# Optimization experiments

Measured on AMD Instinct MI355X. Metric: run time of the kernel, lower is better.

The kernel has to match this reference:

```python
import jax, jax.numpy as jnp
import numpy as np

N = 2048      # num_nodes
K = 8         # Chebyshev order
HEADS = 4
BETA = 0.5
EPS = 1e-6


def setup_inputs() -> dict:
    key = jax.random.key(0)
    ks = jax.random.split(key, 5)
    # edge_index enumerates all ordered node pairs i != j (row-major), matching
    # the [2, N*(N-1)] logits parameter layout of the module.
    ii, jj = np.meshgrid(np.arange(N), np.arange(N), indexing='ij')
    mask = ii != jj
    edge_index = jnp.asarray(np.stack([ii[mask], jj[mask]]), dtype=jnp.int32)  # [2, E]
    E = N * (N - 1)
    logits = jax.random.normal(ks[0], (2, E), dtype=jnp.float32)
    s = 1.0 / np.sqrt(K)
    w0 = jax.random.normal(ks[1], (HEADS, K), dtype=jnp.float32) * s  # Linear(K,1) weight per head
    b0 = jax.random.normal(ks[2], (HEADS,), dtype=jnp.float32) * s
    w1 = jax.random.normal(ks[3], (HEADS, K), dtype=jnp.float32) * s
    b1 = jax.random.normal(ks[4], (HEADS,), dtype=jnp.float32) * s
    return {"edge_index": edge_index, "logits": logits, "w0": w0, "b0": b0, "w1": w1, "b1": b1}


def _laplacian(vals, src, dst, dtype):
    # to_dense_adj + L = -D^{-1/2} A D^{-1/2}, with diag matmuls as broadcast scaling
    A = jnp.zeros((N, N), dtype).at[src, dst].add(vals)
    dinv = 1.0 / jnp.sqrt(A.sum(axis=1) + EPS)
    return -(dinv[:, None] * A) * dinv[None, :]


def _cheb_gather(L, src, dst):
    # T1 = L, Tk = 2 L Tkm1 - Tkm2; gather edge entries of T1..TK -> [E, K]
    cols = [L[src, dst]]
    Tkm2 = jnp.eye(N, dtype=L.dtype)
    Tkm1 = L
    for _ in range(K - 1):
        Tk = 2.0 * (L @ Tkm1) - Tkm2
        cols.append(Tk[src, dst])
        Tkm2, Tkm1 = Tkm1, Tk
    return jnp.stack(cols, axis=1)


def reference(edge_index, logits, w0, b0, w1, b1):
    src, dst = edge_index[0], edge_index[1]
    edge_prob = jax.nn.softmax(BETA * logits, axis=0)  # softmax over the 2 branches
    L0 = _laplacian(edge_prob[0], src, dst, logits.dtype)
    L1 = _laplacian(edge_prob[1], src, dst, logits.dtype)
    Lks0 = _cheb_gather(L0, src, dst)  # [E, K]
    Lks1 = _cheb_gather(L1, src, dst)  # [E, K]
    f0 = (Lks0 @ w0.T + b0).T  # [heads, E], theta0[i](Lks0).squeeze(-1)
    f1 = (Lks1 @ w1.T + b1).T  # [heads, E]
    return edge_prob, f0, f1
```

## Files before the change

### kernel.cpp

```cpp
#include <hip/hip_runtime.h>
#include <math.h>

#define NN 2048
#define NM1 2047
#define EDGES (NN * NM1)
#define KORD 8
#define NHEADS 4
#define BETA 0.5f
#define EPSV 1e-6f

typedef __attribute__((ext_vector_type(8))) short bf16x8;
typedef __attribute__((ext_vector_type(4))) float f32x4;

__device__ __forceinline__ unsigned short f2bf(float f) {
    unsigned u = __builtin_bit_cast(unsigned, f);
    u += 0x7FFF + ((u >> 16) & 1);
    return (unsigned short)(u >> 16);
}
__device__ __forceinline__ float bf2f(unsigned short h) {
    unsigned u = ((unsigned)h) << 16;
    return __builtin_bit_cast(float, u);
}

#define GLD16(gp, lp) __builtin_amdgcn_global_load_lds(                         \
    (const __attribute__((address_space(1))) void*)(gp),                        \
    (__attribute__((address_space(3))) void*)(lp), 16, 0, 0)

__global__ void k_prob(const float* __restrict__ logits, float* __restrict__ out) {
    int e = blockIdx.x * 256 + threadIdx.x;
    if (e >= EDGES) return;
    float l0 = logits[e];
    float l1 = logits[EDGES + e];
    float p0 = 1.f / (1.f + __expf(BETA * (l1 - l0)));
    float p1 = 1.f / (1.f + __expf(BETA * (l0 - l1)));
    out[e]         = p0;
    out[EDGES + e] = p1;
}

__global__ __launch_bounds__(256) void k_dinv(const float* __restrict__ out, float* __restrict__ dinv) {
    int row = blockIdx.x, br = blockIdx.y;
    const float* p = out + (size_t)br * EDGES + (size_t)row * NM1;
    float s = 0.f;
    for (int t = threadIdx.x; t < NM1; t += 256) s += p[t];
    for (int off = 32; off; off >>= 1) s += __shfl_down(s, off);
    __shared__ float red[4];
    if ((threadIdx.x & 63) == 0) red[threadIdx.x >> 6] = s;
    __syncthreads();
    if (threadIdx.x == 0)
        dinv[br * NN + row] = 1.f / sqrtf(red[0] + red[1] + red[2] + red[3] + EPSV);
}

__global__ __launch_bounds__(256) void k_build(const float* __restrict__ out, const float* __restrict__ dinv,
                                               unsigned short* __restrict__ Lb0, unsigned short* __restrict__ Lb1) {
    int idx = blockIdx.x * 256 + threadIdx.x;
    int br = blockIdx.y;
    int i = idx >> 11, j = idx & (NN - 1);
    unsigned short* Lb = br ? Lb1 : Lb0;
    float v = 0.f;
    if (i != j) {
        float pp = out[(size_t)br * EDGES + (size_t)i * NM1 + (j < i ? j : j - 1)];
        v = -dinv[br * NN + i] * pp * dinv[br * NN + j];
    }
    Lb[idx] = f2bf(v);
}

__global__ __launch_bounds__(256) void k_transpose(
    const unsigned short* __restrict__ S0, const unsigned short* __restrict__ S1,
    unsigned short* __restrict__ D0, unsigned short* __restrict__ D1) {
    __shared__ unsigned short T[64 * 66];
    const unsigned short* S = blockIdx.z ? S1 : S0;
    unsigned short* D = blockIdx.z ? D1 : D0;
    int t = threadIdx.x;
    int I0 = blockIdx.y * 64, J0 = blockIdx.x * 64;
    int r = t >> 2, cb = (t & 3) * 16;
    {
        const uint4* src = (const uint4*)(S + (size_t)(I0 + r) * NN + J0 + cb);
        uint4 v0 = src[0], v1 = src[1];
        unsigned* d = (unsigned*)&T[r * 66 + cb];
        d[0] = v0.x; d[1] = v0.y; d[2] = v0.z; d[3] = v0.w;
        d[4] = v1.x; d[5] = v1.y; d[6] = v1.z; d[7] = v1.w;
    }
    __syncthreads();
    union { unsigned short u[16]; uint4 q[2]; } pk;
#pragma unroll
    for (int q = 0; q < 16; ++q) pk.u[q] = T[(cb + q) * 66 + r];
    unsigned short* dst = D + (size_t)(J0 + r) * NN + I0 + cb;
    ((uint4*)dst)[0] = pk.q[0];
    ((uint4*)dst)[1] = pk.q[1];
}

__global__ __launch_bounds__(256) void k_cheb(
    const unsigned short* __restrict__ A0, const unsigned short* __restrict__ A1,
    const unsigned short* __restrict__ B0, const unsigned short* __restrict__ B1,
    const unsigned short* __restrict__ P0, const unsigned short* __restrict__ P1,
    unsigned short* __restrict__ O0, unsigned short* __restrict__ O1, int first) {
    __shared__ unsigned short As[128 * 32];
    __shared__ unsigned short Bs[128 * 32];
    const int z = blockIdx.z;
    const unsigned short* A   = z ? A1 : A0;
    const unsigned short* BT  = z ? B1 : B0;
    const unsigned short* Um2 = z ? P1 : P0;
    unsigned short* Un        = z ? O1 : O0;

    int tid = threadIdx.x;
    int w = tid >> 6, l = tid & 63;
    int wr = w >> 1, wc = w & 1;
    int r0 = blockIdx.y * 128, c0 = blockIdx.x * 128;

    int srow = l >> 2;
    int schk = ((l & 3) ^ ((l >> 3) & 3)) * 8;
    const unsigned short* ga  = A  + (size_t)(r0 + w * 16 + srow) * NN + schk;
    const unsigned short* gb  = BT + (size_t)(c0 + w * 16 + srow) * NN + schk;
    const unsigned short* ga2 = ga + (size_t)64 * NN;
    const unsigned short* gb2 = gb + (size_t)64 * NN;
    unsigned short* lA  = As + w * 512;
    unsigned short* lA2 = As + 2048 + w * 512;
    unsigned short* lB  = Bs + w * 512;
    unsigned short* lB2 = Bs + 2048 + w * 512;

    f32x4 acc[4][4] = {};
    int lr = l & 15, g = l >> 4;
    int rchk = (g ^ ((lr >> 1) & 3)) * 8;

    for (int k0 = 0; k0 < NN; k0 += 32) {
        __syncthreads();
        GLD16(ga + k0, lA);
        GLD16(ga2 + k0, lA2);
        GLD16(gb + k0, lB);
        GLD16(gb2 + k0, lB2);
        __syncthreads();
        bf16x8 af[4], bf[4];
#pragma unroll
        for (int m = 0; m < 4; ++m)
            af[m] = *(const bf16x8*)(As + (wr * 64 + m * 16 + lr) * 32 + rchk);
#pragma unroll
        for (int n = 0; n < 4; ++n)
            bf[n] = *(const bf16x8*)(Bs + (wc * 64 + n * 16 + lr) * 32 + rchk);
#pragma unroll
        for (int m = 0; m < 4; ++m)
#pragma unroll
            for (int n = 0; n < 4; ++n)
                acc[m][n] = __builtin_amdgcn_mfma_f32_16x16x32_bf16(af[m], bf[n], acc[m][n], 0, 0, 0);
    }

#pragma unroll
    for (int m = 0; m < 4; ++m)
#pragma unroll
        for (int n = 0; n < 4; ++n)
#pragma unroll
            for (int r = 0; r < 4; ++r) {
                int row = r0 + wr * 64 + m * 16 + g * 4 + r;
                int col = c0 + wc * 64 + n * 16 + lr;
                size_t off = (size_t)row * NN + col;
                float prev = first ? (row == col ? 1.f : 0.f) : bf2f(Um2[off]);
                Un[off] = f2bf(2.f * acc[m][n][r] - prev);
            }
}

__global__ __launch_bounds__(256) void k_gather(
    const unsigned short* __restrict__ Lb,
    const unsigned short* __restrict__ U2, const unsigned short* __restrict__ U3,
    const unsigned short* __restrict__ U4, const unsigned short* __restrict__ U5,
    const unsigned short* __restrict__ U6, const unsigned short* __restrict__ U7,
    const unsigned short* __restrict__ U8,
    const float* __restrict__ w, const float* __restrict__ bias,
    float* __restrict__ fout) {
    __shared__ unsigned short G[64 * 66];
    int t = threadIdx.x;
    int I0 = blockIdx.y * 64, J0 = blockIdx.x * 64;
    int jo = t & 63, ig = t >> 6;
    int sr = t >> 2, scb = (t & 3) * 16;

    float acc[4][16];
#pragma unroll
    for (int h = 0; h < 4; ++h)
#pragma unroll
        for (int s = 0; s < 16; ++s) acc[h][s] = 0.f;

    const unsigned short* mats[8] = {Lb, U2, U3, U4, U5, U6, U7, U8};
#pragma unroll
    for (int kk = 0; kk < 8; ++kk) {
        const unsigned short* M = mats[kk];
        int R0 = (kk == 0) ? I0 : J0;
        int C0 = (kk == 0) ? J0 : I0;
        __syncthreads();
        {
            const uint4* src = (const uint4*)(M + (size_t)(R0 + sr) * NN + C0 + scb);
            uint4 v0 = src[0], v1 = src[1];
            unsigned* d = (unsigned*)&G[sr * 66 + scb];
            d[0] = v0.x; d[1] = v0.y; d[2] = v0.z; d[3] = v0.w;
            d[4] = v1.x; d[5] = v1.y; d[6] = v1.z; d[7] = v1.w;
        }
        __syncthreads();
        float c0w = w[0 * KORD + kk], c1w = w[1 * KORD + kk];
        float c2w = w[2 * KORD + kk], c3w = w[3 * KORD + kk];
#pragma unroll
        for (int s = 0; s < 16; ++s) {
            int io = ig * 16 + s;
            unsigned short raw = (kk == 0) ? G[io * 66 + jo] : G[jo * 66 + io];
            float v = bf2f(raw);
            acc[0][s] += c0w * v;
            acc[1][s] += c1w * v;
            acc[2][s] += c2w * v;
            acc[3][s] += c3w * v;
        }
    }
    float b0v = bias[0], b1v = bias[1], b2v = bias[2], b3v = bias[3];
#pragma unroll
    for (int s = 0; s < 16; ++s) {
        int i = I0 + ig * 16 + s;
        int j = J0 + jo;
        if (i == j) continue;
        size_t e = (size_t)i * NM1 + (j < i ? j : j - 1);
        fout[0 * (size_t)EDGES + e] = b0v + acc[0][s];
        fout[1 * (size_t)EDGES + e] = b1v + acc[1][s];
        fout[2 * (size_t)EDGES + e] = b2v + acc[2][s];
        fout[3 * (size_t)EDGES + e] = b3v + acc[3][s];
    }
}

extern "C" void kernel_launch(void* const* d_in, const int* in_sizes, int n_in,
                              void* d_out, int out_size, void* d_ws, size_t ws_size,
                              hipStream_t stream) {
    const float* logits = (const float*)d_in[1];
    const float* w0 = (const float*)d_in[2];
    const float* b0 = (const float*)d_in[3];
    const float* w1 = (const float*)d_in[4];
    const float* b1 = (const float*)d_in[5];
    float* out = (float*)d_out;

    char* ws = (char*)d_ws;
    const size_t MATB = (size_t)NN * NN * sizeof(unsigned short);
    unsigned short* Lb0 = (unsigned short*)(ws);
    unsigned short* Lb1 = (unsigned short*)(ws + MATB);
    unsigned short* U0[9];
    for (int k = 2; k <= 8; ++k) U0[k] = (unsigned short*)(ws + (size_t)k * MATB);
    float* dinv = (float*)(ws + 9 * MATB);
    unsigned short* obase = (unsigned short*)(out + 2 * (size_t)EDGES);
    unsigned short* U1[9];
    for (int k = 2; k <= 8; ++k) U1[k] = obase + (size_t)(k - 2) * NN * NN;
    unsigned short* LT0 = U0[8];
    unsigned short* LT1 = U1[8];

    k_prob<<<(EDGES + 255) / 256, 256, 0, stream>>>(logits, out);
    k_dinv<<<dim3(NN, 2), 256, 0, stream>>>(out, dinv);
    k_build<<<dim3((NN * NN) / 256, 2), 256, 0, stream>>>(out, dinv, Lb0, Lb1);
    k_transpose<<<dim3(32, 32, 2), 256, 0, stream>>>(Lb0, Lb1, LT0, LT1);

    for (int n = 2; n <= 8; ++n) {
        const unsigned short* A0p = (n == 2) ? LT0 : U0[n - 1];
        const unsigned short* A1p = (n == 2) ? LT1 : U1[n - 1];
        const unsigned short* P0p = (n <= 3) ? LT0 : U0[n - 2];
        const unsigned short* P1p = (n <= 3) ? LT1 : U1[n - 2];
        k_cheb<<<dim3(16, 16, 2), 256, 0, stream>>>(A0p, A1p, Lb0, Lb1, P0p, P1p,
                                                    U0[n], U1[n], (n == 2) ? 1 : 0);
    }

    float* f1 = out + 2 * (size_t)EDGES + 4 * (size_t)EDGES;
    k_gather<<<dim3(32, 32), 256, 0, stream>>>(Lb1, U1[2], U1[3], U1[4], U1[5], U1[6], U1[7], U1[8],
                                               w1, b1, f1);
    float* f0 = out + 2 * (size_t)EDGES;
    k_gather<<<dim3(32, 32), 256, 0, stream>>>(Lb0, U0[2], U0[3], U0[4], U0[5], U0[6], U0[7], U0[8],
                                               w0, b0, f0);
}
```

Measured before the change: 696.1 us.

## Use Chebyshev product identity to compute two orders per GEMM launch

Result: faster. 617.1 us (-11.4%).

```diff
diff --git a/kernel.cpp b/kernel.cpp
--- a/kernel.cpp
+++ b/kernel.cpp
@@ -37,31 +37,40 @@
     out[EDGES + e] = p1;
 }
 
-__global__ __launch_bounds__(256) void k_dinv(const float* __restrict__ out, float* __restrict__ dinv) {
-    int row = blockIdx.x, br = blockIdx.y;
-    const float* p = out + (size_t)br * EDGES + (size_t)row * NM1;
+__global__ __launch_bounds__(256) void k_dinv(const float* __restrict__ logits, float* __restrict__ dinv) {
+    int row = blockIdx.x;
+    const float* r0 = logits + (size_t)row * NM1;
+    const float* r1 = r0 + EDGES;
     float s = 0.f;
-    for (int t = threadIdx.x; t < NM1; t += 256) s += p[t];
+    for (int t = threadIdx.x; t < NM1; t += 256) {
+        float l0 = r0[t], l1 = r1[t];
+        s += 1.f / (1.f + __expf(BETA * (l1 - l0)));
+    }
     for (int off = 32; off; off >>= 1) s += __shfl_down(s, off);
     __shared__ float red[4];
     if ((threadIdx.x & 63) == 0) red[threadIdx.x >> 6] = s;
     __syncthreads();
-    if (threadIdx.x == 0)
-        dinv[br * NN + row] = 1.f / sqrtf(red[0] + red[1] + red[2] + red[3] + EPSV);
-}
-
-__global__ __launch_bounds__(256) void k_build(const float* __restrict__ out, const float* __restrict__ dinv,
+    if (threadIdx.x == 0) {
+        float s0 = red[0] + red[1] + red[2] + red[3];
+        dinv[row]      = 1.f / sqrtf(s0 + EPSV);
+        dinv[NN + row] = 1.f / sqrtf((float)NM1 - s0 + EPSV);
+    }
+}
+
+__global__ __launch_bounds__(256) void k_build(const float* __restrict__ logits, const float* __restrict__ dinv,
                                                unsigned short* __restrict__ Lb0, unsigned short* __restrict__ Lb1) {
     int idx = blockIdx.x * 256 + threadIdx.x;
-    int br = blockIdx.y;
     int i = idx >> 11, j = idx & (NN - 1);
-    unsigned short* Lb = br ? Lb1 : Lb0;
-    float v = 0.f;
+    float v0 = 0.f, v1 = 0.f;
     if (i != j) {
-        float pp = out[(size_t)br * EDGES + (size_t)i * NM1 + (j < i ? j : j - 1)];
-        v = -dinv[br * NN + i] * pp * dinv[br * NN + j];
-    }
-    Lb[idx] = f2bf(v);
+        size_t e = (size_t)i * NM1 + (j < i ? j : j - 1);
+        float l0 = logits[e], l1 = logits[EDGES + e];
+        float p0 = 1.f / (1.f + __expf(BETA * (l1 - l0)));
+        v0 = -dinv[i] * p0 * dinv[j];
+        v1 = -dinv[NN + i] * (1.f - p0) * dinv[NN + j];
+    }
+    Lb0[idx] = f2bf(v0);
+    Lb1[idx] = f2bf(v1);
 }
 
 __global__ __launch_bounds__(256) void k_transpose(
@@ -89,23 +98,16 @@
     ((uint4*)dst)[1] = pk.q[1];
 }
 
-__global__ __launch_bounds__(256) void k_cheb(
-    const unsigned short* __restrict__ A0, const unsigned short* __restrict__ A1,
-    const unsigned short* __restrict__ B0, const unsigned short* __restrict__ B1,
-    const unsigned short* __restrict__ P0, const unsigned short* __restrict__ P1,
-    unsigned short* __restrict__ O0, unsigned short* __restrict__ O1, int first) {
+__device__ __forceinline__ void gemm_core(
+    const unsigned short* __restrict__ A, const unsigned short* __restrict__ BT,
+    const unsigned short* __restrict__ Um2, unsigned short* __restrict__ Un,
+    int first, int r0, int c0) {
     __shared__ unsigned short As[128 * 32];
     __shared__ unsigned short Bs[128 * 32];
-    const int z = blockIdx.z;
-    const unsigned short* A   = z ? A1 : A0;
-    const unsigned short* BT  = z ? B1 : B0;
-    const unsigned short* Um2 = z ? P1 : P0;
-    unsigned short* Un        = z ? O1 : O0;
 
     int tid = threadIdx.x;
     int w = tid >> 6, l = tid & 63;
     int wr = w >> 1, wc = w & 1;
-    int r0 = blockIdx.y * 128, c0 = blockIdx.x * 128;
 
     int srow = l >> 2;
     int schk = ((l & 3) ^ ((l >> 3) & 3)) * 8;
@@ -157,12 +159,38 @@
             }
 }
 
+__global__ __launch_bounds__(256, 4) void k_cheb1(
+    const unsigned short* __restrict__ LT0, const unsigned short* __restrict__ LT1,
+    const unsigned short* __restrict__ Lb0, const unsigned short* __restrict__ Lb1,
+    unsigned short* __restrict__ U20, unsigned short* __restrict__ U21) {
+    int z = blockIdx.z;
+    gemm_core(z ? LT1 : LT0, z ? Lb1 : Lb0, z ? LT1 : LT0, z ? U21 : U20, 1,
+              blockIdx.y * 128, blockIdx.x * 128);
+}
+
+__global__ __launch_bounds__(256, 4) void k_chebp(
+    const unsigned short* __restrict__ Alo0, const unsigned short* __restrict__ Ahi0,
+    const unsigned short* __restrict__ Alo1, const unsigned short* __restrict__ Ahi1,
+    const unsigned short* __restrict__ BT0,  const unsigned short* __restrict__ BT1,
+    const unsigned short* __restrict__ Plo0, const unsigned short* __restrict__ Phi0,
+    const unsigned short* __restrict__ Plo1, const unsigned short* __restrict__ Phi1,
+    unsigned short* __restrict__ Olo0, unsigned short* __restrict__ Ohi0,
+    unsigned short* __restrict__ Olo1, unsigned short* __restrict__ Ohi1,
+    int firstlo, int firsthi) {
+    int z = blockIdx.z;
+    int half = blockIdx.y >> 4, my = blockIdx.y & 15;
+    const unsigned short* A  = z ? (half ? Ahi1 : Alo1) : (half ? Ahi0 : Alo0);
+    const unsigned short* BT = z ? BT1 : BT0;
+    const unsigned short* P  = z ? (half ? Phi1 : Plo1) : (half ? Phi0 : Plo0);
+    unsigned short* O        = z ? (half ? Ohi1 : Olo1) : (half ? Ohi0 : Olo0);
+    gemm_core(A, BT, P, O, half ? firsthi : firstlo, my * 128, blockIdx.x * 128);
+}
+
 __global__ __launch_bounds__(256) void k_gather(
-    const unsigned short* __restrict__ Lb,
-    const unsigned short* __restrict__ U2, const unsigned short* __restrict__ U3,
-    const unsigned short* __restrict__ U4, const unsigned short* __restrict__ U5,
-    const unsigned short* __restrict__ U6, const unsigned short* __restrict__ U7,
-    const unsigned short* __restrict__ U8,
+    const unsigned short* __restrict__ M1, const unsigned short* __restrict__ M2,
+    const unsigned short* __restrict__ M3, const unsigned short* __restrict__ M4,
+    const unsigned short* __restrict__ M5, const unsigned short* __restrict__ M6,
+    const unsigned short* __restrict__ M7, const unsigned short* __restrict__ M8,
     const float* __restrict__ w, const float* __restrict__ bias,
     float* __restrict__ fout) {
     __shared__ unsigned short G[64 * 66];
@@ -177,15 +205,13 @@
 #pragma unroll
         for (int s = 0; s < 16; ++s) acc[h][s] = 0.f;
 
-    const unsigned short* mats[8] = {Lb, U2, U3, U4, U5, U6, U7, U8};
+    const unsigned short* mats[8] = {M1, M2, M3, M4, M5, M6, M7, M8};
 #pragma unroll
     for (int kk = 0; kk < 8; ++kk) {
         const unsigned short* M = mats[kk];
-        int R0 = (kk == 0) ? I0 : J0;
-        int C0 = (kk == 0) ? J0 : I0;
         __syncthreads();
         {
-            const uint4* src = (const uint4*)(M + (size_t)(R0 + sr) * NN + C0 + scb);
+            const uint4* src = (const uint4*)(M + (size_t)(J0 + sr) * NN + I0 + scb);
             uint4 v0 = src[0], v1 = src[1];
             unsigned* d = (unsigned*)&G[sr * 66 + scb];
             d[0] = v0.x; d[1] = v0.y; d[2] = v0.z; d[3] = v0.w;
@@ -197,8 +223,7 @@
 #pragma unroll
         for (int s = 0; s < 16; ++s) {
             int io = ig * 16 + s;
-            unsigned short raw = (kk == 0) ? G[io * 66 + jo] : G[jo * 66 + io];
-            float v = bf2f(raw);
+            float v = bf2f(G[jo * 66 + io]);
             acc[0][s] += c0w * v;
             acc[1][s] += c1w * v;
             acc[2][s] += c2w * v;
@@ -229,37 +254,40 @@
     const float* b1 = (const float*)d_in[5];
     float* out = (float*)d_out;
 
+    const size_t MATB = (size_t)NN * NN * sizeof(unsigned short);
     char* ws = (char*)d_ws;
-    const size_t MATB = (size_t)NN * NN * sizeof(unsigned short);
-    unsigned short* Lb0 = (unsigned short*)(ws);
-    unsigned short* Lb1 = (unsigned short*)(ws + MATB);
-    unsigned short* U0[9];
-    for (int k = 2; k <= 8; ++k) U0[k] = (unsigned short*)(ws + (size_t)k * MATB);
+    unsigned short* s0[9];
+    for (int k = 0; k < 9; ++k) s0[k] = (unsigned short*)(ws + (size_t)k * MATB);
     float* dinv = (float*)(ws + 9 * MATB);
-    unsigned short* obase = (unsigned short*)(out + 2 * (size_t)EDGES);
-    unsigned short* U1[9];
-    for (int k = 2; k <= 8; ++k) U1[k] = obase + (size_t)(k - 2) * NN * NN;
-    unsigned short* LT0 = U0[8];
-    unsigned short* LT1 = U1[8];
-
-    k_prob<<<(EDGES + 255) / 256, 256, 0, stream>>>(logits, out);
-    k_dinv<<<dim3(NN, 2), 256, 0, stream>>>(out, dinv);
-    k_build<<<dim3((NN * NN) / 256, 2), 256, 0, stream>>>(out, dinv, Lb0, Lb1);
-    k_transpose<<<dim3(32, 32, 2), 256, 0, stream>>>(Lb0, Lb1, LT0, LT1);
-
-    for (int n = 2; n <= 8; ++n) {
-        const unsigned short* A0p = (n == 2) ? LT0 : U0[n - 1];
-        const unsigned short* A1p = (n == 2) ? LT1 : U1[n - 1];
-        const unsigned short* P0p = (n <= 3) ? LT0 : U0[n - 2];
-        const unsigned short* P1p = (n <= 3) ? LT1 : U1[n - 2];
-        k_cheb<<<dim3(16, 16, 2), 256, 0, stream>>>(A0p, A1p, Lb0, Lb1, P0p, P1p,
-                                                    U0[n], U1[n], (n == 2) ? 1 : 0);
-    }
-
-    float* f1 = out + 2 * (size_t)EDGES + 4 * (size_t)EDGES;
-    k_gather<<<dim3(32, 32), 256, 0, stream>>>(Lb1, U1[2], U1[3], U1[4], U1[5], U1[6], U1[7], U1[8],
+    char* ob = (char*)d_out;
+    unsigned short* s1[9];
+    for (int k = 0; k < 9; ++k) s1[k] = (unsigned short*)(ob + (size_t)k * MATB);
+
+    k_dinv<<<NN, 256, 0, stream>>>(logits, dinv);
+    k_build<<<(NN * NN) / 256, 256, 0, stream>>>(logits, dinv, s0[0], s1[0]);
+    k_transpose<<<dim3(32, 32, 2), 256, 0, stream>>>(s0[0], s1[0], s0[1], s1[1]);
+
+    k_cheb1<<<dim3(16, 16, 2), 256, 0, stream>>>(s0[1], s1[1], s0[0], s1[0], s0[2], s1[2]);
+    k_transpose<<<dim3(32, 32, 2), 256, 0, stream>>>(s0[2], s1[2], s0[0], s1[0]);
+
+    k_chebp<<<dim3(16, 32, 2), 256, 0, stream>>>(
+        s0[1], s0[2], s1[1], s1[2], s0[0], s1[0],
+        s0[1], s0[2], s1[1], s1[2],
+        s0[3], s0[4], s1[3], s1[4], 0, 1);
+    k_chebp<<<dim3(16, 32, 2), 256, 0, stream>>>(
+        s0[3], s0[4], s1[3], s1[4], s0[0], s1[0],
+        s0[1], s0[2], s1[1], s1[2],
+        s0[5], s0[6], s1[5], s1[6], 0, 0);
+    k_chebp<<<dim3(16, 32, 2), 256, 0, stream>>>(
+        s0[5], s0[6], s1[5], s1[6], s0[0], s1[0],
+        s0[3], s0[4], s1[3], s1[4],
+        s0[7], s0[8], s1[7], s1[8], 0, 0);
+
+    float* f1 = out + 6 * (size_t)EDGES;
+    k_gather<<<dim3(32, 32), 256, 0, stream>>>(s1[1], s1[2], s1[3], s1[4], s1[5], s1[6], s1[7], s1[8],
                                                w1, b1, f1);
     float* f0 = out + 2 * (size_t)EDGES;
-    k_gather<<<dim3(32, 32), 256, 0, stream>>>(Lb0, U0[2], U0[3], U0[4], U0[5], U0[6], U0[7], U0[8],
+    k_gather<<<dim3(32, 32), 256, 0, stream>>>(s0[1], s0[2], s0[3], s0[4], s0[5], s0[6], s0[7], s0[8],
                                                w0, b0, f0);
-}
+    k_prob<<<(EDGES + 255) / 256, 256, 0, stream>>>(logits, out);
+}
```
